# Optimization experiments

Hardware: AMD Instinct MI355X
Metric: run time of the kernel (lower is better)

The kernel has to match this reference:

```python
import jax, jax.numpy as jnp
import numpy as np

L, BS, H, W, C, NH = 6, 2, 48, 192, 128, 8
DIM = C // NH
EPS_LN = 1e-5
EPS_LA = 1e-6


def layer_norm(x, g, b):
    m = x.mean(-1, keepdims=True)
    v = ((x - m) ** 2).mean(-1, keepdims=True)
    return (x - m) / jnp.sqrt(v + EPS_LN) * g + b


def lin(x, w):
    # torch nn.Linear convention: y = x @ W^T
    return jnp.einsum('...i,oi->...o', x, w)


def linear_attention(q, k, v):
    # LoFTR-style kernelized attention: phi(x) = elu(x) + 1
    Q = jax.nn.elu(q) + 1.0
    K = jax.nn.elu(k) + 1.0
    KV = jnp.einsum('nshd,nshv->nhdv', K, v)            # [n, nh, d, d]
    Z = 1.0 / (jnp.einsum('nlhd,nhd->nlh', Q, K.sum(1)) + EPS_LA)
    return jnp.einsum('nlhd,nhdv,nlh->nlhv', Q, KV, Z)  # [n, l, nh, d]


def full_attention(q, k, v):
    scale = 1.0 / np.sqrt(q.shape[-1])
    qk = jnp.einsum('nlhd,nshd->nlsh', q, k) * scale    # [n, l, s, nh]
    A = jax.nn.softmax(qk, axis=2)
    out = jnp.einsum('nlsh,nshd->nlhd', A, v)
    return out, A


def self_layer(x, p):
    bs, h, w, c = x.shape
    xf = x.reshape(bs, h * w, c)
    xn = layer_norm(xf, p['n1_g'], p['n1_b'])
    q = lin(xn, p['q']).reshape(bs, h * w, NH, DIM)
    k = lin(xn, p['k']).reshape(bs, h * w, NH, DIM)
    v = lin(xn, p['v']).reshape(bs, h * w, NH, DIM)
    msg = linear_attention(q, k, v).reshape(bs, h * w, c)
    msg = xf + lin(msg, p['merge'])
    mn = layer_norm(msg, p['n2_g'], p['n2_b'])
    mn = lin(jax.nn.gelu(lin(mn, p['mlp1']), approximate=False), p['mlp2'])
    return (msg + mn).reshape(bs, h, w, c)


def cross_layer(fl, fr, p):
    bs, h, w, c = fl.shape
    fln = layer_norm(fl, p['n1_g'], p['n1_b'])
    frn = layer_norm(fr, p['n1_g'], p['n1_b'])

    def proj(x, wm):
        return lin(x, wm).reshape(bs * h, w, NH, DIM)

    ql, kl, vl = proj(fln, p['q']), proj(fln, p['k']), proj(fln, p['v'])
    qr, kr, vr = proj(frn, p['q']), proj(frn, p['k']), proj(frn, p['v'])

    def half(feat, q, k, v):
        msg, A = full_attention(q, k, v)
        raw = A.sum(-1).reshape(bs, h, w, w)
        m = feat + lin(msg.reshape(bs, h, w, c), p['merge'])
        mn = layer_norm(m, p['n2_g'], p['n2_b'])
        mn = lin(jax.nn.gelu(lin(mn, p['mlp1']), approximate=False), p['mlp2'])
        return m + mn, raw

    ml, raw_l = half(fl, ql, kr, vr)
    mr, raw_r = half(fr, qr, kl, vl)
    return ml, mr, raw_l, raw_r


PARAM_NAMES = ['q', 'k', 'v', 'merge', 'mlp1', 'mlp2']
VEC_NAMES = ['n1_g', 'n1_b', 'n2_g', 'n2_b']


def setup_inputs() -> dict:
    key = jax.random.key(0)
    ks = jax.random.split(key, 16)
    s = 1.0 / np.sqrt(C)
    inp = {
        'feat_left': jax.random.normal(ks[0], (BS, H, W, C), jnp.float32),
        'feat_right': jax.random.normal(ks[1], (BS, H, W, C), jnp.float32),
        'attn_left': jnp.zeros((BS, H, W, W), jnp.float32),
        'attn_right': jnp.zeros((BS, H, W, W), jnp.float32),
    }
    for i, nm in enumerate(PARAM_NAMES):
        inp['sa_' + nm] = jax.random.normal(ks[2 + i], (L, C, C), jnp.float32) * s
        inp['ca_' + nm] = jax.random.normal(ks[8 + i], (L, C, C), jnp.float32) * s
    for nm in VEC_NAMES:
        fill = jnp.ones if nm.endswith('_g') else jnp.zeros
        inp['sa_' + nm] = fill((L, C), jnp.float32)
        inp['ca_' + nm] = fill((L, C), jnp.float32)
    return inp


def reference(feat_left, feat_right, attn_left, attn_right,
              sa_q, sa_k, sa_v, sa_merge, sa_mlp1, sa_mlp2,
              sa_n1_g, sa_n1_b, sa_n2_g, sa_n2_b,
              ca_q, ca_k, ca_v, ca_merge, ca_mlp1, ca_mlp2,
              ca_n1_g, ca_n1_b, ca_n2_g, ca_n2_b):
    sa = {'q': sa_q, 'k': sa_k, 'v': sa_v, 'merge': sa_merge, 'mlp1': sa_mlp1,
          'mlp2': sa_mlp2, 'n1_g': sa_n1_g, 'n1_b': sa_n1_b, 'n2_g': sa_n2_g, 'n2_b': sa_n2_b}
    ca = {'q': ca_q, 'k': ca_k, 'v': ca_v, 'merge': ca_merge, 'mlp1': ca_mlp1,
          'mlp2': ca_mlp2, 'n1_g': ca_n1_g, 'n1_b': ca_n1_b, 'n2_g': ca_n2_g, 'n2_b': ca_n2_b}
    fl, fr, al, ar = feat_left, feat_right, attn_left, attn_right
    for i in range(L):
        p_sa = {k_: v_[i] for k_, v_ in sa.items()}
        p_ca = {k_: v_[i] for k_, v_ in ca.items()}
        fl = self_layer(fl, p_sa)
        fr = self_layer(fr, p_sa)
        fl, fr, raw_l, raw_r = cross_layer(fl, fr, p_ca)
        al = al + raw_l
        ar = ar + raw_r
    return fl, fr, (al, ar)
```

## Files before the change

kernel.cpp:

```cpp
#include <hip/hip_runtime.h>
#include <hip/hip_bf16.h>

using bf16x8 = __attribute__((ext_vector_type(8))) short;
using bf16x4 = __attribute__((ext_vector_type(4))) short;
using f32x4  = __attribute__((ext_vector_type(4))) float;

#define NE      4718592
#define HALF_R  18432
#define ATTN_E  3538944
#define SEQ     9216
#define NCHUNK  18
#define VSTRIDE 3088

typedef const unsigned int __attribute__((address_space(1)))* gas_u32;
typedef unsigned int __attribute__((address_space(3)))* las_u32;

__device__ __forceinline__ float b2f(short s) {
  union { unsigned u; float f; } x; x.u = ((unsigned)(unsigned short)s) << 16; return x.f;
}
__device__ __forceinline__ short f2b(float f) {
  __hip_bfloat16 h = __float2bfloat16(f);
  short s; __builtin_memcpy(&s, &h, 2); return s;
}
__device__ __forceinline__ f32x4 mfma16(bf16x8 a, bf16x8 b, f32x4 c) {
  return __builtin_amdgcn_mfma_f32_16x16x32_bf16(a, b, c, 0, 0, 0);
}
__device__ __forceinline__ f32x4 mfma16k16(bf16x4 a, bf16x4 b, f32x4 c) {
#if __has_builtin(__builtin_amdgcn_mfma_f32_16x16x16bf16_1k)
  return __builtin_amdgcn_mfma_f32_16x16x16bf16_1k(a, b, c, 0, 0, 0);
#else
  f32x4 d;
  asm("v_mfma_f32_16x16x16_bf16 %0, %1, %2, %3" : "=v"(d) : "v"(a), "v"(b), "v"(c));
  return d;
#endif
}

#define TR_READ12(V0,V1,V2,V3,V4,V5,V6,V7,V8,V9,V10,V11, ADDR) \
  asm volatile( \
    "ds_read_b64_tr_b16 %0, %12 offset:0\n\t" \
    "ds_read_b64_tr_b16 %1, %12 offset:512\n\t" \
    "ds_read_b64_tr_b16 %2, %12 offset:1024\n\t" \
    "ds_read_b64_tr_b16 %3, %12 offset:1536\n\t" \
    "ds_read_b64_tr_b16 %4, %12 offset:2048\n\t" \
    "ds_read_b64_tr_b16 %5, %12 offset:2560\n\t" \
    "ds_read_b64_tr_b16 %6, %12 offset:3072\n\t" \
    "ds_read_b64_tr_b16 %7, %12 offset:3584\n\t" \
    "ds_read_b64_tr_b16 %8, %12 offset:4096\n\t" \
    "ds_read_b64_tr_b16 %9, %12 offset:4608\n\t" \
    "ds_read_b64_tr_b16 %10, %12 offset:5120\n\t" \
    "ds_read_b64_tr_b16 %11, %12 offset:5632\n\t" \
    "s_waitcnt lgkmcnt(0)" \
    : "=&v"(V0), "=&v"(V1), "=&v"(V2), "=&v"(V3), "=&v"(V4), "=&v"(V5), \
      "=&v"(V6), "=&v"(V7), "=&v"(V8), "=&v"(V9), "=&v"(V10), "=&v"(V11) \
    : "v"(ADDR))

__global__ void k_copy(const float* __restrict__ in, float* __restrict__ out, int n) {
  for (int i = blockIdx.x*blockDim.x + threadIdx.x; i < n; i += gridDim.x*blockDim.x)
    out[i] = in[i];
}
__global__ void k_zero(float* __restrict__ p, int n) {
  for (int i = blockIdx.x*blockDim.x + threadIdx.x; i < n; i += gridDim.x*blockDim.x)
    p[i] = 0.f;
}
__global__ void k_addf(const float* __restrict__ base, const float* __restrict__ acc,
                       float* __restrict__ out, int n) {
  for (int i = blockIdx.x*blockDim.x + threadIdx.x; i < n; i += gridDim.x*blockDim.x)
    out[i] = base[i] + acc[i];
}
__global__ void k_w2b(const float* s0, const float* s1, const float* s2, const float* s3,
                      const float* s4, const float* s5, const float* s6, const float* s7,
                      const float* s8, const float* s9, const float* s10, const float* s11,
                      short* __restrict__ dst) {
  const float* srcs[12] = {s0,s1,s2,s3,s4,s5,s6,s7,s8,s9,s10,s11};
  const float* src = srcs[blockIdx.y];
  short* d = dst + (size_t)blockIdx.y*6*16384;
  int idx = blockIdx.x*256 + threadIdx.x;
  int layer = idx >> 11, w = idx & 2047;
  int c = w >> 4, gp = w & 15;
  int gs = gp ^ (c & 7);
  const float* s = src + layer*16384 + c*128 + gs*8;
  f32x4 v0 = *(const f32x4*)(s);
  f32x4 v1 = *(const f32x4*)(s + 4);
  short tmp[8];
  tmp[0]=f2b(v0[0]); tmp[1]=f2b(v0[1]); tmp[2]=f2b(v0[2]); tmp[3]=f2b(v0[3]);
  tmp[4]=f2b(v1[0]); tmp[5]=f2b(v1[1]); tmp[6]=f2b(v1[2]); tmp[7]=f2b(v1[3]);
  bf16x8 pk; __builtin_memcpy(&pk, tmp, 16);
  *(bf16x8*)(d + layer*16384 + c*128 + gp*8) = pk;
}

__device__ __forceinline__ void stage_W_async(const short* __restrict__ Wt, short* Ws,
                                              int wave, int lane) {
  #pragma unroll
  for (int is = 0; is < 8; is++) {
    int chunk = is*4 + wave;
    __builtin_amdgcn_global_load_lds((gas_u32)(const void*)(Wt + chunk*512 + lane*8),
                                     (las_u32)(void*)(Ws + chunk*512), 16, 0, 0);
  }
}
__device__ __forceinline__ void mfma_core_regA(const bf16x8 af[4], const short* Ws,
                                               int lane, f32x4 acc[8]) {
  int lrow = lane & 15, lgrp = lane >> 4;
  #pragma unroll
  for (int ct = 0; ct < 8; ct++) {
    int c = ct*16 + lrow;
    #pragma unroll
    for (int kc = 0; kc < 4; kc++) {
      int g = (kc*4 + lgrp) ^ (c & 7);
      bf16x8 wf = *(const bf16x8*)(&Ws[c*128 + g*8]);
      acc[ct] = mfma16(wf, af[kc], acc[ct]);
    }
  }
}
__device__ __forceinline__ void mfma_core_T(const short* As, const short* Ws,
                                            int wave, int lane, f32x4 acc[8]) {
  int lrow = lane & 15, lgrp = lane >> 4;
  bf16x8 af[4];
  int rl = wave*16 + lrow;
  #pragma unroll
  for (int kc = 0; kc < 4; kc++) {
    int g = (kc*4 + lgrp) ^ (rl & 7);
    af[kc] = *(const bf16x8*)(&As[rl*128 + g*8]);
  }
  mfma_core_regA(af, Ws, lane, acc);
}

__global__ __launch_bounds__(256) void k_qkv3(const float* __restrict__ F,
                                              const short* __restrict__ Wq,
                                              const short* __restrict__ Wk,
                                              const short* __restrict__ Wv,
                                              const float* __restrict__ g,
                                              const float* __restrict__ b,
                                              short* __restrict__ Qo,
                                              short* __restrict__ Ko,
                                              short* __restrict__ Vo,
                                              int phi_mask, float qscale) {
  __shared__ short Ws[128*128];
  int tid = threadIdx.x;
  int row0 = blockIdx.x * 64;
  int wave = tid >> 6, lane = tid & 63;
  int lrow = lane & 15, lgrp = lane >> 4;
  int rl = wave*16 + lrow;
  int row = row0 + rl;
  stage_W_async(Wq, Ws, wave, lane);
  float x[4][8];
  const float* fr = F + (size_t)row*128;
  #pragma unroll
  for (int kc = 0; kc < 4; kc++) {
    f32x4 v0 = *(const f32x4*)(fr + kc*32 + lgrp*8);
    f32x4 v1 = *(const f32x4*)(fr + kc*32 + lgrp*8 + 4);
    x[kc][0]=v0[0]; x[kc][1]=v0[1]; x[kc][2]=v0[2]; x[kc][3]=v0[3];
    x[kc][4]=v1[0]; x[kc][5]=v1[1]; x[kc][6]=v1[2]; x[kc][7]=v1[3];
  }
  float s = 0.f, sq = 0.f;
  #pragma unroll
  for (int kc = 0; kc < 4; kc++)
    #pragma unroll
    for (int j = 0; j < 8; j++) { float xx = x[kc][j]; s += xx; sq += xx*xx; }
  s += __shfl_xor(s, 16, 64); sq += __shfl_xor(sq, 16, 64);
  s += __shfl_xor(s, 32, 64); sq += __shfl_xor(sq, 32, 64);
  float mean = s * (1.f/128.f);
  float var  = sq * (1.f/128.f) - mean*mean;
  float inv  = rsqrtf(var + 1e-5f);
  bf16x8 af[4];
  #pragma unroll
  for (int kc = 0; kc < 4; kc++) {
    int c0 = kc*32 + lgrp*8;
    f32x4 g0 = *(const f32x4*)(g + c0), g1 = *(const f32x4*)(g + c0 + 4);
    f32x4 b0 = *(const f32x4*)(b + c0), b1 = *(const f32x4*)(b + c0 + 4);
    short t8[8];
    t8[0]=f2b((x[kc][0]-mean)*inv*g0[0]+b0[0]); t8[1]=f2b((x[kc][1]-mean)*inv*g0[1]+b0[1]);
    t8[2]=f2b((x[kc][2]-mean)*inv*g0[2]+b0[2]); t8[3]=f2b((x[kc][3]-mean)*inv*g0[3]+b0[3]);
    t8[4]=f2b((x[kc][4]-mean)*inv*g1[0]+b1[0]); t8[5]=f2b((x[kc][5]-mean)*inv*g1[1]+b1[1]);
    t8[6]=f2b((x[kc][6]-mean)*inv*g1[2]+b1[2]); t8[7]=f2b((x[kc][7]-mean)*inv*g1[3]+b1[3]);
    __builtin_memcpy(&af[kc], t8, 16);
  }
  const short* Wp[3] = {Wq, Wk, Wv};
  short* Op[3] = {Qo, Ko, Vo};
  for (int y = 0; y < 3; y++) {
    __syncthreads();
    f32x4 acc[8] = {};
    mfma_core_regA(af, Ws, lane, acc);
    bool phi = (phi_mask >> y) & 1;
    float sc = (y == 0) ? qscale : 1.0f;
    short* OUT = Op[y] + (size_t)row*128 + lgrp*4;
    __syncthreads();
    if (y < 2) stage_W_async(Wp[y+1], Ws, wave, lane);
    #pragma unroll
    for (int ct = 0; ct < 8; ct++) {
      short t4[4];
      #pragma unroll
      for (int reg = 0; reg < 4; reg++) {
        float v = acc[ct][reg] * sc;
        if (phi) v = (v > 0.f) ? v + 1.0f : __expf(v);
        t4[reg] = f2b(v);
      }
      bf16x4 pk; __builtin_memcpy(&pk, t4, 8);
      *(bf16x4*)(OUT + ct*16) = pk;
    }
  }
}

template<bool REGA>
__device__ __forceinline__ void mlp_tail(const bf16x8 af1[4], short* As, short* Ws,
                                         const short* __restrict__ W1,
                                         const short* __restrict__ W2,
                                         const float* __restrict__ g,
                                         const float* __restrict__ b,
                                         float* __restrict__ F, int row0, int tid) {
  int wave = tid >> 6, lane = tid & 63;
  int lrow = lane & 15, lgrp = lane >> 4;
  int rl = wave*16 + lrow;
  int orow = row0 + rl;
  float* Frow = F + (size_t)orow*128 + lgrp*4;
  f32x4 acc[8] = {};
  if (REGA) mfma_core_regA(af1, Ws, lane, acc);
  else      mfma_core_T(As, Ws, wave, lane, acc);
  f32x4 fnew[8];
  #pragma unroll
  for (int ct = 0; ct < 8; ct++) {
    f32x4 fv = *(const f32x4*)(Frow + ct*16);
    fnew[ct] = acc[ct] + fv;
  }
  float s = 0.f, sq = 0.f;
  #pragma unroll
  for (int ct = 0; ct < 8; ct++)
    #pragma unroll
    for (int reg = 0; reg < 4; reg++) { float x = fnew[ct][reg]; s += x; sq += x*x; }
  s += __shfl_xor(s, 16, 64); sq += __shfl_xor(sq, 16, 64);
  s += __shfl_xor(s, 32, 64); sq += __shfl_xor(sq, 32, 64);
  float mean = s * (1.f/128.f);
  float var  = sq * (1.f/128.f) - mean*mean;
  float inv  = rsqrtf(var + 1e-5f);
  __syncthreads();
  stage_W_async(W1, Ws, wave, lane);
  #pragma unroll
  for (int ct = 0; ct < 8; ct++) {
    short t4[4];
    #pragma unroll
    for (int reg = 0; reg < 4; reg++) {
      int c = ct*16 + lgrp*4 + reg;
      t4[reg] = f2b((fnew[ct][reg] - mean) * inv * g[c] + b[c]);
    }
    bf16x4 pk; __builtin_memcpy(&pk, t4, 8);
    int G = ct*2 + (lgrp >> 1);
    *(bf16x4*)(&As[rl*128 + ((G ^ (rl & 7))*8) + (lgrp & 1)*4]) = pk;
  }
  __syncthreads();
  f32x4 acc2[8] = {};
  mfma_core_T(As, Ws, wave, lane, acc2);
  __syncthreads();
  stage_W_async(W2, Ws, wave, lane);
  #pragma unroll
  for (int ct = 0; ct < 8; ct++) {
    short t4[4];
    #pragma unroll
    for (int reg = 0; reg < 4; reg++) {
      float v = acc2[ct][reg];
      v = 0.5f*v*(1.0f + erff(v*0.70710678118654752f));
      t4[reg] = f2b(v);
    }
    bf16x4 pk; __builtin_memcpy(&pk, t4, 8);
    int G = ct*2 + (lgrp >> 1);
    *(bf16x4*)(&As[rl*128 + ((G ^ (rl & 7))*8) + (lgrp & 1)*4]) = pk;
  }
  __syncthreads();
  f32x4 acc3[8] = {};
  mfma_core_T(As, Ws, wave, lane, acc3);
  #pragma unroll
  for (int ct = 0; ct < 8; ct++) {
    f32x4 o = fnew[ct] + acc3[ct];
    *(f32x4*)(Frow + ct*16) = o;
  }
}

__global__ __launch_bounds__(256) void k_mlp(const short* __restrict__ Msg,
                                             const short* __restrict__ Wm,
                                             const short* __restrict__ W1,
                                             const short* __restrict__ W2,
                                             const float* __restrict__ g,
                                             const float* __restrict__ b,
                                             float* __restrict__ F) {
  __shared__ short As[64*128];
  __shared__ short Ws[128*128];
  int tid = threadIdx.x;
  int row0 = blockIdx.x * 64;
  int wave = tid >> 6, lane = tid & 63;
  int lrow = lane & 15, lgrp = lane >> 4;
  int row = row0 + wave*16 + lrow;
  stage_W_async(Wm, Ws, wave, lane);
  bf16x8 af1[4];
  const short* mr = Msg + (size_t)row*128;
  #pragma unroll
  for (int kc = 0; kc < 4; kc++)
    af1[kc] = *(const bf16x8*)(mr + kc*32 + lgrp*8);
  __syncthreads();
  mlp_tail<true>(af1, As, Ws, W1, W2, g, b, F, row0, tid);
}

__global__ __launch_bounds__(256) void k_mlp_self(const short* __restrict__ Q,
                                                  const float* __restrict__ kvp,
                                                  const short* __restrict__ Wm,
                                                  const short* __restrict__ W1,
                                                  const short* __restrict__ W2,
                                                  const float* __restrict__ g,
                                                  const float* __restrict__ b,
                                                  float* __restrict__ F) {
  __shared__ short As[64*128];
  __shared__ short Ws[128*128];
  __shared__ float kvs[8*272];
  int tid = threadIdx.x;
  int row0 = blockIdx.x * 64;
  int n = row0 / SEQ;
  stage_W_async(Wm, Ws, tid >> 6, tid & 63);
  for (int i = tid; i < 8*272; i += 256) {
    int h = i / 272, j = i % 272;
    const float* src = kvp + ((size_t)(n*8 + h)*NCHUNK)*272 + j;
    float s = 0.f;
    #pragma unroll
    for (int c2 = 0; c2 < NCHUNK; c2++) s += src[(size_t)c2*272];
    kvs[i] = s;
  }
  __syncthreads();
  int r = tid >> 2, qq = tid & 3;
  const short* qr = Q + (size_t)(row0 + r)*128;
  #pragma unroll
  for (int hh = 0; hh < 2; hh++) {
    int h = qq*2 + hh;
    bf16x8 q0 = *(const bf16x8*)(qr + h*16);
    bf16x8 q1 = *(const bf16x8*)(qr + h*16 + 8);
    float q[16];
    #pragma unroll
    for (int j = 0; j < 8; j++) { q[j] = b2f(q0[j]); q[8+j] = b2f(q1[j]); }
    const float* kvh = kvs + h*272;
    float z = 1e-6f;
    #pragma unroll
    for (int d = 0; d < 16; d++) z += q[d] * kvh[256 + d];
    float invz = 1.f / z;
    short o16[16];
    #pragma unroll
    for (int d2 = 0; d2 < 16; d2++) {
      float o = 0.f;
      #pragma unroll
      for (int d = 0; d < 16; d++) o += q[d] * kvh[d*16 + d2];
      o16[d2] = f2b(o * invz);
    }
    bf16x8 lo, hi; __builtin_memcpy(&lo, o16, 16); __builtin_memcpy(&hi, o16+8, 16);
    *(bf16x8*)(&As[r*128 + (((2*h)   ^ (r & 7))*8)]) = lo;
    *(bf16x8*)(&As[r*128 + (((2*h+1) ^ (r & 7))*8)]) = hi;
  }
  __syncthreads();
  mlp_tail<false>(nullptr, As, Ws, W1, W2, g, b, F, row0, tid);
}

__global__ __launch_bounds__(256) void k_linred(const short* __restrict__ K,
                                                const short* __restrict__ V,
                                                float* __restrict__ kvp) {
  int nh = blockIdx.x;
  int n = nh >> 3, h = nh & 7;
  int chunk = blockIdx.y;
  int r0 = chunk * (SEQ / NCHUNK);
  __shared__ float ks[64][17], vs[64][17];
  int tid = threadIdx.x;
  int d1 = tid >> 4, d2 = tid & 15;
  int rr = tid >> 2, q = tid & 3;
  float kv = 0.f, ksum = 0.f;
  for (int r = r0; r < r0 + SEQ/NCHUNK; r += 64) {
    __syncthreads();
    bf16x4 kk = *(const bf16x4*)(K + (size_t)(n*SEQ + r + rr)*128 + h*16 + q*4);
    bf16x4 vv = *(const bf16x4*)(V + (size_t)(n*SEQ + r + rr)*128 + h*16 + q*4);
    #pragma unroll
    for (int j = 0; j < 4; j++) { ks[rr][q*4+j] = b2f(kk[j]); vs[rr][q*4+j] = b2f(vv[j]); }
    __syncthreads();
    #pragma unroll
    for (int j = 0; j < 64; j++) {
      float kvl = ks[j][d1];
      kv   += kvl * vs[j][d2];
      ksum += kvl;
    }
  }
  float* dst = kvp + ((size_t)nh*NCHUNK + chunk)*272;
  dst[d1*16 + d2] = kv;
  if (d2 == 0) dst[256 + d1] = ksum;
}

__global__ __launch_bounds__(256) void k_fullattn(const short* __restrict__ Q,
                                                  const short* __restrict__ K,
                                                  const short* __restrict__ V,
                                                  short* __restrict__ MSG,
                                                  float* __restrict__ AL,
                                                  float* __restrict__ AR) {
  __shared__ __attribute__((aligned(16))) char smem[8*VSTRIDE*2];
  short* Vsub = (short*)smem;
  float* rawb = (float*)smem;
  int side = blockIdx.y;
  int bx = blockIdx.x;
  int n = bx >> 2, part = bx & 3;
  int qbase = side*HALF_R + n*192;
  int kbase = (side^1)*HALF_R + n*192;
  float* rawbase = (side ? AR : AL) + (size_t)n*192*192;
  int tid = threadIdx.x;
  int wave = tid >> 6, lane = tid & 63;
  int lrow = lane & 15, lgrp = lane >> 4;

  #pragma unroll
  for (int i = 0; i < 12; i++) {
    int c = tid + 256*i;
    int s = c >> 4, t8 = c & 15;
    bf16x8 v8 = *(const bf16x8*)(V + (size_t)(kbase + s)*128 + t8*8);
    *(bf16x8*)(&Vsub[(t8 >> 1)*VSTRIDE + s*16 + (t8 & 1)*8]) = v8;
  }
  __syncthreads();

  bf16x4 vf[2][12];
  {
    unsigned base = (unsigned)(uintptr_t)(&Vsub[0]) + lane*8;
    unsigned va0 = base + (wave*2 + 0)*(VSTRIDE*2);
    unsigned va1 = base + (wave*2 + 1)*(VSTRIDE*2);
    TR_READ12(vf[0][0], vf[0][1], vf[0][2], vf[0][3], vf[0][4], vf[0][5],
              vf[0][6], vf[0][7], vf[0][8], vf[0][9], vf[0][10], vf[0][11], va0);
    TR_READ12(vf[1][0], vf[1][1], vf[1][2], vf[1][3], vf[1][4], vf[1][5],
              vf[1][6], vf[1][7], vf[1][8], vf[1][9], vf[1][10], vf[1][11], va1);
  }
  __builtin_amdgcn_sched_barrier(0);
  bf16x4 kfr[2][12];
  #pragma unroll
  for (int hh = 0; hh < 2; hh++)
    #pragma unroll
    for (int st = 0; st < 12; st++)
      kfr[hh][st] = *(const bf16x4*)(K + (size_t)(kbase + st*16 + lrow)*128
                                       + (wave*2 + hh)*16 + lgrp*4);
  __syncthreads();

  const f32x4 z4 = {0.f, 0.f, 0.f, 0.f};
  for (int li = 0; li < 3; li++) {
    int l0 = (part*3 + li)*16;
    #pragma unroll
    for (int hh = 0; hh < 2; hh++) {
      int h = wave*2 + hh;
      bf16x4 qf = *(const bf16x4*)(Q + (size_t)(qbase + l0 + lrow)*128 + h*16 + lgrp*4);
      f32x4 sa[12];
      #pragma unroll
      for (int st = 0; st < 12; st++)
        sa[st] = mfma16k16(kfr[hh][st], qf, z4);
      float m = -1e30f;
      #pragma unroll
      for (int st = 0; st < 12; st++)
        m = fmaxf(m, fmaxf(fmaxf(sa[st][0], sa[st][1]), fmaxf(sa[st][2], sa[st][3])));
      m = fmaxf(m, __shfl_xor(m, 16, 64));
      m = fmaxf(m, __shfl_xor(m, 32, 64));
      float sum = 0.f;
      #pragma unroll
      for (int st = 0; st < 12; st++) {
        #pragma unroll
        for (int r = 0; r < 4; r++) {
          float p = __expf(sa[st][r] - m);
          sa[st][r] = p; sum += p;
        }
      }
      sum += __shfl_xor(sum, 16, 64);
      sum += __shfl_xor(sum, 32, 64);
      float inv = 1.f / sum;
      #pragma unroll
      for (int st = 0; st < 12; st++) {
        sa[st][0] *= inv; sa[st][1] *= inv; sa[st][2] *= inv; sa[st][3] *= inv;
      }
      #pragma unroll
      for (int st = 0; st < 12; st++) {
        f32x4* slot = (f32x4*)(&rawb[(((wave*12) + st)*64 + lane)*4]);
        if (hh == 0) *slot = sa[st];
        else         *slot = *slot + sa[st];
      }
      f32x4 o = z4;
      #pragma unroll
      for (int st = 0; st < 12; st++) {
        bf16x4 pf;
        pf[0] = f2b(sa[st][0]); pf[1] = f2b(sa[st][1]);
        pf[2] = f2b(sa[st][2]); pf[3] = f2b(sa[st][3]);
        o = mfma16k16(vf[hh][st], pf, o);
      }
      bf16x4 o4;
      o4[0] = f2b(o[0]); o4[1] = f2b(o[1]); o4[2] = f2b(o[2]); o4[3] = f2b(o[3]);
      *(bf16x4*)(MSG + (size_t)(qbase + l0 + lrow)*128 + h*16 + lgrp*4) = o4;
    }
    __syncthreads();
    #pragma unroll
    for (int i = 0; i < 3; i++) {
      int slot = tid + 256*i;
      int st = slot >> 6, p = slot & 63;
      f32x4 a = *(const f32x4*)(&rawb[((0*12 + st)*64 + p)*4]);
      f32x4 b = *(const f32x4*)(&rawb[((1*12 + st)*64 + p)*4]);
      f32x4 c = *(const f32x4*)(&rawb[((2*12 + st)*64 + p)*4]);
      f32x4 d = *(const f32x4*)(&rawb[((3*12 + st)*64 + p)*4]);
      f32x4 t = (a + b) + (c + d);
      float* gp = rawbase + (size_t)(l0 + (p & 15))*192 + st*16 + ((p >> 4)*4);
      f32x4 cur = *(const f32x4*)gp;
      *(f32x4*)gp = cur + t;
    }
    __syncthreads();
  }
}

extern "C" void kernel_launch(void* const* d_in, const int* in_sizes, int n_in,
                              void* d_out, int out_size, void* d_ws, size_t ws_size,
                              hipStream_t stream) {
  const float* feat_l = (const float*)d_in[0];
  const float* feat_r = (const float*)d_in[1];
  const float* attn_l = (const float*)d_in[2];
  const float* attn_r = (const float*)d_in[3];
  const float* saw[6] = { (const float*)d_in[4],  (const float*)d_in[6],  (const float*)d_in[8],
                          (const float*)d_in[10], (const float*)d_in[12], (const float*)d_in[14] };
  const float* caw[6] = { (const float*)d_in[5],  (const float*)d_in[7],  (const float*)d_in[9],
                          (const float*)d_in[11], (const float*)d_in[13], (const float*)d_in[15] };
  const float* sa_n1g = (const float*)d_in[16]; const float* ca_n1g = (const float*)d_in[17];
  const float* sa_n1b = (const float*)d_in[18]; const float* ca_n1b = (const float*)d_in[19];
  const float* sa_n2g = (const float*)d_in[20]; const float* ca_n2g = (const float*)d_in[21];
  const float* sa_n2b = (const float*)d_in[22]; const float* ca_n2b = (const float*)d_in[23];

  float* F   = (float*)d_ws;
  float* ALa = F + NE;
  float* ARa = ALa + ATTN_E;
  float* KVp = ARa + ATTN_E;
  short* WB  = (short*)(KVp + 32*NCHUNK*272);
  short* Qb  = WB + 12*6*16384;
  short* Kb  = Qb + NE;
  short* Vb  = Kb + NE;
  short* Mb  = Vb + NE;

  k_w2b<<<dim3(48,12), 256, 0, stream>>>(saw[0],saw[1],saw[2],saw[3],saw[4],saw[5],
                                         caw[0],caw[1],caw[2],caw[3],caw[4],caw[5], WB);
  k_copy<<<1024, 256, 0, stream>>>(feat_l, F, NE/2);
  k_copy<<<1024, 256, 0, stream>>>(feat_r, F + NE/2, NE/2);
  k_zero<<<2048, 256, 0, stream>>>(ALa, 2*ATTN_E);

  for (int i = 0; i < 6; i++) {
    const short* sw[6], *cw[6];
    for (int t = 0; t < 6; t++) { sw[t] = WB + (size_t)(t*6 + i)*16384; cw[t] = WB + (size_t)((6+t)*6 + i)*16384; }
    int vo = i*128;
    k_qkv3<<<576, 256, 0, stream>>>(F, sw[0], sw[1], sw[2], sa_n1g+vo, sa_n1b+vo,
                                    Qb, Kb, Vb, 0b011, 1.0f);
    k_linred<<<dim3(32, NCHUNK), 256, 0, stream>>>(Kb, Vb, KVp);
    k_mlp_self<<<576, 256, 0, stream>>>(Qb, KVp, sw[3], sw[4], sw[5],
                                        sa_n2g+vo, sa_n2b+vo, F);
    k_qkv3<<<576, 256, 0, stream>>>(F, cw[0], cw[1], cw[2], ca_n1g+vo, ca_n1b+vo,
                                    Qb, Kb, Vb, 0, 0.25f);
    k_fullattn<<<dim3(384, 2), 256, 0, stream>>>(Qb, Kb, Vb, Mb, ALa, ARa);
    k_mlp<<<576, 256, 0, stream>>>(Mb, cw[3], cw[4], cw[5], ca_n2g+vo, ca_n2b+vo, F);
  }

  float* out = (float*)d_out;
  k_copy<<<2048, 256, 0, stream>>>(F, out, NE);
  k_addf<<<2048, 256, 0, stream>>>(attn_l, ALa, out + NE, ATTN_E);
  k_addf<<<2048, 256, 0, stream>>>(attn_r, ARa, out + NE + ATTN_E, ATTN_E);
}
```

Before: 1.051 ms.

## Use one wave per head in full attention with 512-thread blocks

The cross-attention kernel now runs 8 waves per block, one per head, where before 4 waves each looped over two heads. This halves the per-wave register arrays for the K and V fragments and adds parallelism per block, with the aim of better latency hiding. In exchange, the cross-head sum of attention probabilities needs an extra shared-memory pass and an extra barrier, since waves 4-7 add into slots written by waves 0-3. The launch bound now asks for 512 threads with a minimum of 4 blocks per CU, which may force register spilling.

```diff
diff --git a/kernel.cpp b/kernel.cpp
--- a/kernel.cpp
+++ b/kernel.cpp
@@ -285,8 +285,8 @@
   int tid = threadIdx.x;
   int row0 = blockIdx.x * 64;
   int wave = tid >> 6, lane = tid & 63;
-  int lrow = lane & 15, lgrp = lane >> 4;
-  int row = row0 + wave*16 + lrow;
+  int lgrp = lane >> 4;
+  int row = row0 + wave*16 + (lane & 15);
   stage_W_async(Wm, Ws, wave, lane);
   bf16x8 af1[4];
   const short* mr = Msg + (size_t)row*128;
@@ -383,12 +383,12 @@
   if (d2 == 0) dst[256 + d1] = ksum;
 }
 
-__global__ __launch_bounds__(256) void k_fullattn(const short* __restrict__ Q,
-                                                  const short* __restrict__ K,
-                                                  const short* __restrict__ V,
-                                                  short* __restrict__ MSG,
-                                                  float* __restrict__ AL,
-                                                  float* __restrict__ AR) {
+__global__ __launch_bounds__(512, 4) void k_fullattn(const short* __restrict__ Q,
+                                                     const short* __restrict__ K,
+                                                     const short* __restrict__ V,
+                                                     short* __restrict__ MSG,
+                                                     float* __restrict__ AL,
+                                                     float* __restrict__ AR) {
   __shared__ __attribute__((aligned(16))) char smem[8*VSTRIDE*2];
   short* Vsub = (short*)smem;
   float* rawb = (float*)smem;
@@ -403,98 +403,100 @@
   int lrow = lane & 15, lgrp = lane >> 4;
 
   #pragma unroll
-  for (int i = 0; i < 12; i++) {
-    int c = tid + 256*i;
+  for (int i = 0; i < 6; i++) {
+    int c = tid + 512*i;
     int s = c >> 4, t8 = c & 15;
     bf16x8 v8 = *(const bf16x8*)(V + (size_t)(kbase + s)*128 + t8*8);
     *(bf16x8*)(&Vsub[(t8 >> 1)*VSTRIDE + s*16 + (t8 & 1)*8]) = v8;
   }
   __syncthreads();
 
-  bf16x4 vf[2][12];
+  bf16x4 vf[12];
   {
-    unsigned base = (unsigned)(uintptr_t)(&Vsub[0]) + lane*8;
-    unsigned va0 = base + (wave*2 + 0)*(VSTRIDE*2);
-    unsigned va1 = base + (wave*2 + 1)*(VSTRIDE*2);
-    TR_READ12(vf[0][0], vf[0][1], vf[0][2], vf[0][3], vf[0][4], vf[0][5],
-              vf[0][6], vf[0][7], vf[0][8], vf[0][9], vf[0][10], vf[0][11], va0);
-    TR_READ12(vf[1][0], vf[1][1], vf[1][2], vf[1][3], vf[1][4], vf[1][5],
-              vf[1][6], vf[1][7], vf[1][8], vf[1][9], vf[1][10], vf[1][11], va1);
+    unsigned va = (unsigned)(uintptr_t)(&Vsub[0]) + wave*(VSTRIDE*2) + lane*8;
+    TR_READ12(vf[0], vf[1], vf[2], vf[3], vf[4], vf[5],
+              vf[6], vf[7], vf[8], vf[9], vf[10], vf[11], va);
   }
   __builtin_amdgcn_sched_barrier(0);
-  bf16x4 kfr[2][12];
-  #pragma unroll
-  for (int hh = 0; hh < 2; hh++)
-    #pragma unroll
-    for (int st = 0; st < 12; st++)
-      kfr[hh][st] = *(const bf16x4*)(K + (size_t)(kbase + st*16 + lrow)*128
-                                       + (wave*2 + hh)*16 + lgrp*4);
+  bf16x4 kfr[12];
+  #pragma unroll
+  for (int st = 0; st < 12; st++)
+    kfr[st] = *(const bf16x4*)(K + (size_t)(kbase + st*16 + lrow)*128
+                                 + wave*16 + lgrp*4);
   __syncthreads();
 
   const f32x4 z4 = {0.f, 0.f, 0.f, 0.f};
+  int g = wave & 3;
   for (int li = 0; li < 3; li++) {
     int l0 = (part*3 + li)*16;
-    #pragma unroll
-    for (int hh = 0; hh < 2; hh++) {
-      int h = wave*2 + hh;
-      bf16x4 qf = *(const bf16x4*)(Q + (size_t)(qbase + l0 + lrow)*128 + h*16 + lgrp*4);
-      f32x4 sa[12];
+    bf16x4 qf = *(const bf16x4*)(Q + (size_t)(qbase + l0 + lrow)*128 + wave*16 + lgrp*4);
+    f32x4 sa[12];
+    #pragma unroll
+    for (int st = 0; st < 12; st++)
+      sa[st] = mfma16k16(kfr[st], qf, z4);
+    float m = -1e30f;
+    #pragma unroll
+    for (int st = 0; st < 12; st++)
+      m = fmaxf(m, fmaxf(fmaxf(sa[st][0], sa[st][1]), fmaxf(sa[st][2], sa[st][3])));
+    m = fmaxf(m, __shfl_xor(m, 16, 64));
+    m = fmaxf(m, __shfl_xor(m, 32, 64));
+    float sum = 0.f;
+    #pragma unroll
+    for (int st = 0; st < 12; st++) {
       #pragma unroll
-      for (int st = 0; st < 12; st++)
-        sa[st] = mfma16k16(kfr[hh][st], qf, z4);
-      float m = -1e30f;
-      #pragma unroll
-      for (int st = 0; st < 12; st++)
-        m = fmaxf(m, fmaxf(fmaxf(sa[st][0], sa[st][1]), fmaxf(sa[st][2], sa[st][3])));
-      m = fmaxf(m, __shfl_xor(m, 16, 64));
-      m = fmaxf(m, __shfl_xor(m, 32, 64));
-      float sum = 0.f;
-      #pragma unroll
-      for (int st = 0; st < 12; st++) {
-        #pragma unroll
-        for (int r = 0; r < 4; r++) {
-          float p = __expf(sa[st][r] - m);
-          sa[st][r] = p; sum += p;
-        }
+      for (int r = 0; r < 4; r++) {
+        float p = __expf(sa[st][r] - m);
+        sa[st][r] = p; sum += p;
       }
-      sum += __shfl_xor(sum, 16, 64);
-      sum += __shfl_xor(sum, 32, 64);
-      float inv = 1.f / sum;
-      #pragma unroll
-      for (int st = 0; st < 12; st++) {
-        sa[st][0] *= inv; sa[st][1] *= inv; sa[st][2] *= inv; sa[st][3] *= inv;
-      }
-      #pragma unroll
-      for (int st = 0; st < 12; st++) {
-        f32x4* slot = (f32x4*)(&rawb[(((wave*12) + st)*64 + lane)*4]);
-        if (hh == 0) *slot = sa[st];
-        else         *slot = *slot + sa[st];
-      }
+    }
+    sum += __shfl_xor(sum, 16, 64);
+    sum += __shfl_xor(sum, 32, 64);
+    float inv = 1.f / sum;
+    #pragma unroll
+    for (int st = 0; st < 12; st++) {
+      sa[st][0] *= inv; sa[st][1] *= inv; sa[st][2] *= inv; sa[st][3] *= inv;
+    }
+    {
       f32x4 o = z4;
       #pragma unroll
       for (int st = 0; st < 12; st++) {
         bf16x4 pf;
         pf[0] = f2b(sa[st][0]); pf[1] = f2b(sa[st][1]);
         pf[2] = f2b(sa[st][2]); pf[3] = f2b(sa[st][3]);
-        o = mfma16k16(vf[hh][st], pf, o);
+        o = mfma16k16(vf[st], pf, o);
       }
       bf16x4 o4;
       o4[0] = f2b(o[0]); o4[1] = f2b(o[1]); o4[2] = f2b(o[2]); o4[3] = f2b(o[3]);
-      *(bf16x4*)(MSG + (size_t)(qbase + l0 + lrow)*128 + h*16 + lgrp*4) = o4;
-    }
-    __syncthreads();
-    #pragma unroll
-    for (int i = 0; i < 3; i++) {
-      int slot = tid + 256*i;
-      int st = slot >> 6, p = slot & 63;
-      f32x4 a = *(const f32x4*)(&rawb[((0*12 + st)*64 + p)*4]);
-      f32x4 b = *(const f32x4*)(&rawb[((1*12 + st)*64 + p)*4]);
-      f32x4 c = *(const f32x4*)(&rawb[((2*12 + st)*64 + p)*4]);
-      f32x4 d = *(const f32x4*)(&rawb[((3*12 + st)*64 + p)*4]);
-      f32x4 t = (a + b) + (c + d);
-      float* gp = rawbase + (size_t)(l0 + (p & 15))*192 + st*16 + ((p >> 4)*4);
-      f32x4 cur = *(const f32x4*)gp;
-      *(f32x4*)gp = cur + t;
+      *(bf16x4*)(MSG + (size_t)(qbase + l0 + lrow)*128 + wave*16 + lgrp*4) = o4;
+    }
+    if (wave < 4) {
+      #pragma unroll
+      for (int st = 0; st < 12; st++)
+        *(f32x4*)(&rawb[(((g*12) + st)*64 + lane)*4]) = sa[st];
+    }
+    __syncthreads();
+    if (wave >= 4) {
+      #pragma unroll
+      for (int st = 0; st < 12; st++) {
+        f32x4* slot = (f32x4*)(&rawb[(((g*12) + st)*64 + lane)*4]);
+        *slot = *slot + sa[st];
+      }
+    }
+    __syncthreads();
+    #pragma unroll
+    for (int i = 0; i < 2; i++) {
+      int slot = tid + 512*i;
+      if (slot < 768) {
+        int st = slot >> 6, p = slot & 63;
+        f32x4 a = *(const f32x4*)(&rawb[((0*12 + st)*64 + p)*4]);
+        f32x4 b = *(const f32x4*)(&rawb[((1*12 + st)*64 + p)*4]);
+        f32x4 c = *(const f32x4*)(&rawb[((2*12 + st)*64 + p)*4]);
+        f32x4 d = *(const f32x4*)(&rawb[((3*12 + st)*64 + p)*4]);
+        f32x4 t = (a + b) + (c + d);
+        float* gp = rawbase + (size_t)(l0 + (p & 15))*192 + st*16 + ((p >> 4)*4);
+        f32x4 cur = *(const f32x4*)gp;
+        *(f32x4*)gp = cur + t;
+      }
     }
     __syncthreads();
   }
@@ -543,7 +545,7 @@
                                         sa_n2g+vo, sa_n2b+vo, F);
     k_qkv3<<<576, 256, 0, stream>>>(F, cw[0], cw[1], cw[2], ca_n1g+vo, ca_n1b+vo,
                                     Qb, Kb, Vb, 0, 0.25f);
-    k_fullattn<<<dim3(384, 2), 256, 0, stream>>>(Qb, Kb, Vb, Mb, ALa, ARa);
+    k_fullattn<<<dim3(384, 2), 512, 0, stream>>>(Qb, Kb, Vb, Mb, ALa, ARa);
     k_mlp<<<576, 256, 0, stream>>>(Mb, cw[3], cw[4], cw[5], ca_n2g+vo, ca_n2b+vo, F);
   }
 
```

Measured after the change: 1.018 ms. -3.2%, faster.
